# Optimization experiments

Hardware: AMD Instinct MI355X
Metric: run time of the kernel (lower is better)

Reference implementation:

```python
import jax, jax.numpy as jnp
import numpy as np


def _bilinear2d(uv, table):
    """Bilinear lookup with wrap addressing; sigmoid non-linearity applied per
    corner (normalize=True in SpatialGrid2D), matching training-time forward.
    uv: (N,2) in [0,1); table: (U,V,L). Returns (N,L)."""
    U, V, _ = table.shape
    su = uv[:, 0] * U
    sv = uv[:, 1] * V
    u0 = jnp.floor(su)
    v0 = jnp.floor(sv)
    fu = (su - u0)[:, None]  # fractional weights, (N,1)
    fv = (sv - v0)[:, None]
    u0i = jnp.mod(u0.astype(jnp.int32), U)
    v0i = jnp.mod(v0.astype(jnp.int32), V)
    u1i = jnp.mod(u0i + 1, U)
    v1i = jnp.mod(v0i + 1, V)
    t00 = jax.nn.sigmoid(table[u0i, v0i])
    t10 = jax.nn.sigmoid(table[u1i, v0i])
    t01 = jax.nn.sigmoid(table[u0i, v1i])
    t11 = jax.nn.sigmoid(table[u1i, v1i])
    return (t00 * (1 - fu) + t10 * fu) * (1 - fv) + (t01 * (1 - fu) + t11 * fu) * fv


def setup_inputs() -> dict:
    key = jax.random.key(0)
    k1, k2, k3 = jax.random.split(key, 3)
    N = 2048 * 2048  # query points (one per pixel)
    RES = 520        # grid0 resolution from nativeResolution=4096, compression=6
    x = jax.random.uniform(k1, (N, 2), dtype=jnp.float32)
    grid1_table = jax.random.normal(k2, (RES * 4, RES * 4, 2), dtype=jnp.float32)
    grid0_table = jax.random.normal(k3, (RES, RES, 3), dtype=jnp.float32)
    return {"x": x, "grid1_table": grid1_table, "grid0_table": grid0_table}


def reference(x, grid1_table, grid0_table):
    # forward: grid0(grid1(x)) -- chained bilinear indirection lookups
    key = _bilinear2d(x, grid1_table)   # (N,2) indirected uv coords in (0,1)
    return _bilinear2d(key, grid0_table)  # (N,3) decoded RGB
```

## Files before the change

### kernel.cpp

```cpp
#include <hip/hip_runtime.h>
#include <math.h>


__device__ __forceinline__ float mul_rn_nocontract(float a, float b) {
    float r;
    asm("v_mul_f32 %0, %1, %2" : "=v"(r) : "v"(a), "v"(b));
    return r;
}

__device__ __forceinline__ float sigmoid_f64(float t) {
    double e = exp(-(double)t);
    return (float)(1.0 / (1.0 + e));
}

__device__ __forceinline__ float sigmoid_fast(float t) {
    return 1.0f / (1.0f + __expf(-t));
}

__global__ void __launch_bounds__(256) sigmoid_table_kernel(
    const float4* __restrict__ in, float4* __restrict__ out, int n4)
{
    int i = blockIdx.x * blockDim.x + threadIdx.x;
    if (i >= n4) return;
    float4 v = in[i];
    float4 r;
    r.x = sigmoid_f64(v.x);
    r.y = sigmoid_f64(v.y);
    r.z = sigmoid_f64(v.z);
    r.w = sigmoid_f64(v.w);
    out[i] = r;
}

__global__ void __launch_bounds__(256) query_kernel(
    const float* __restrict__ x,
    const float* __restrict__ s1,
    const float* __restrict__ s0,
    float* __restrict__ out,
    int N, int U1, int U0)
{
    int i = blockIdx.x * blockDim.x + threadIdx.x;
    if (i >= N) return;

    float2 uv = reinterpret_cast<const float2*>(x)[i];

    float fU1 = (float)U1;
    float su = mul_rn_nocontract(uv.x, fU1);
    float sv = mul_rn_nocontract(uv.y, fU1);
    float u0f = floorf(su), v0f = floorf(sv);
    float fu = su - u0f;
    float fv = sv - v0f;
    int u0 = (int)u0f % U1; if (u0 < 0) u0 += U1;
    int v0 = (int)v0f % U1; if (v0 < 0) v0 += U1;
    int u1 = u0 + 1; if (u1 >= U1) u1 = 0;
    int v1 = v0 + 1; if (v1 >= U1) v1 = 0;

    const float2* s1v = reinterpret_cast<const float2*>(s1);
    float2 t00 = s1v[u0 * U1 + v0];
    float2 t10 = s1v[u1 * U1 + v0];
    float2 t01 = s1v[u0 * U1 + v1];
    float2 t11 = s1v[u1 * U1 + v1];

    float omfu = 1.0f - fu, omfv = 1.0f - fv;
    float kx = (t00.x * omfu + t10.x * fu) * omfv
             + (t01.x * omfu + t11.x * fu) * fv;
    float ky = (t00.y * omfu + t10.y * fu) * omfv
             + (t01.y * omfu + t11.y * fu) * fv;

    float fU0 = (float)U0;
    float su2 = mul_rn_nocontract(kx, fU0);
    float sv2 = mul_rn_nocontract(ky, fU0);
    float u0f2 = floorf(su2), v0f2 = floorf(sv2);
    float fu2 = su2 - u0f2;
    float fv2 = sv2 - v0f2;
    int p0 = (int)u0f2 % U0; if (p0 < 0) p0 += U0;
    int q0 = (int)v0f2 % U0; if (q0 < 0) q0 += U0;
    int p1 = p0 + 1; if (p1 >= U0) p1 = 0;
    int q1 = q0 + 1; if (q1 >= U0) q1 = 0;

    int b00 = (p0 * U0 + q0) * 3;
    int b10 = (p1 * U0 + q0) * 3;
    int b01 = (p0 * U0 + q1) * 3;
    int b11 = (p1 * U0 + q1) * 3;

    float omfu2 = 1.0f - fu2, omfv2 = 1.0f - fv2;

    float r0 = (s0[b00 + 0] * omfu2 + s0[b10 + 0] * fu2) * omfv2
             + (s0[b01 + 0] * omfu2 + s0[b11 + 0] * fu2) * fv2;
    float r1 = (s0[b00 + 1] * omfu2 + s0[b10 + 1] * fu2) * omfv2
             + (s0[b01 + 1] * omfu2 + s0[b11 + 1] * fu2) * fv2;
    float r2 = (s0[b00 + 2] * omfu2 + s0[b10 + 2] * fu2) * omfv2
             + (s0[b01 + 2] * omfu2 + s0[b11 + 2] * fu2) * fv2;

    out[3 * i + 0] = r0;
    out[3 * i + 1] = r1;
    out[3 * i + 2] = r2;
}

__global__ void __launch_bounds__(256) query_kernel_fallback(
    const float* __restrict__ x,
    const float* __restrict__ g1,
    const float* __restrict__ g0,
    float* __restrict__ out,
    int N, int U1, int U0)
{
    int i = blockIdx.x * blockDim.x + threadIdx.x;
    if (i >= N) return;

    float2 uv = reinterpret_cast<const float2*>(x)[i];

    float fU1 = (float)U1;
    float su = mul_rn_nocontract(uv.x, fU1);
    float sv = mul_rn_nocontract(uv.y, fU1);
    float u0f = floorf(su), v0f = floorf(sv);
    float fu = su - u0f, fv = sv - v0f;
    int u0 = (int)u0f % U1; if (u0 < 0) u0 += U1;
    int v0 = (int)v0f % U1; if (v0 < 0) v0 += U1;
    int u1 = u0 + 1; if (u1 >= U1) u1 = 0;
    int v1 = v0 + 1; if (v1 >= U1) v1 = 0;

    const float2* g1v = reinterpret_cast<const float2*>(g1);
    float2 t00 = g1v[u0 * U1 + v0];
    float2 t10 = g1v[u1 * U1 + v0];
    float2 t01 = g1v[u0 * U1 + v1];
    float2 t11 = g1v[u1 * U1 + v1];

    float a00x = sigmoid_f64(t00.x), a00y = sigmoid_f64(t00.y);
    float a10x = sigmoid_f64(t10.x), a10y = sigmoid_f64(t10.y);
    float a01x = sigmoid_f64(t01.x), a01y = sigmoid_f64(t01.y);
    float a11x = sigmoid_f64(t11.x), a11y = sigmoid_f64(t11.y);

    float omfu = 1.0f - fu, omfv = 1.0f - fv;
    float kx = (a00x * omfu + a10x * fu) * omfv + (a01x * omfu + a11x * fu) * fv;
    float ky = (a00y * omfu + a10y * fu) * omfv + (a01y * omfu + a11y * fu) * fv;

    float fU0 = (float)U0;
    float su2 = mul_rn_nocontract(kx, fU0);
    float sv2 = mul_rn_nocontract(ky, fU0);
    float u0f2 = floorf(su2), v0f2 = floorf(sv2);
    float fu2 = su2 - u0f2, fv2 = sv2 - v0f2;
    int p0 = (int)u0f2 % U0; if (p0 < 0) p0 += U0;
    int q0 = (int)v0f2 % U0; if (q0 < 0) q0 += U0;
    int p1 = p0 + 1; if (p1 >= U0) p1 = 0;
    int q1 = q0 + 1; if (q1 >= U0) q1 = 0;

    int b00 = (p0 * U0 + q0) * 3;
    int b10 = (p1 * U0 + q0) * 3;
    int b01 = (p0 * U0 + q1) * 3;
    int b11 = (p1 * U0 + q1) * 3;

    float omfu2 = 1.0f - fu2, omfv2 = 1.0f - fv2;
    float r0 = (sigmoid_fast(g0[b00+0]) * omfu2 + sigmoid_fast(g0[b10+0]) * fu2) * omfv2
             + (sigmoid_fast(g0[b01+0]) * omfu2 + sigmoid_fast(g0[b11+0]) * fu2) * fv2;
    float r1 = (sigmoid_fast(g0[b00+1]) * omfu2 + sigmoid_fast(g0[b10+1]) * fu2) * omfv2
             + (sigmoid_fast(g0[b01+1]) * omfu2 + sigmoid_fast(g0[b11+1]) * fu2) * fv2;
    float r2 = (sigmoid_fast(g0[b00+2]) * omfu2 + sigmoid_fast(g0[b10+2]) * fu2) * omfv2
             + (sigmoid_fast(g0[b01+2]) * omfu2 + sigmoid_fast(g0[b11+2]) * fu2) * fv2;

    out[3 * i + 0] = r0;
    out[3 * i + 1] = r1;
    out[3 * i + 2] = r2;
}

extern "C" void kernel_launch(void* const* d_in, const int* in_sizes, int n_in,
                              void* d_out, int out_size, void* d_ws, size_t ws_size,
                              hipStream_t stream) {
    const float* x  = (const float*)d_in[0];
    const float* g1 = (const float*)d_in[1];
    const float* g0 = (const float*)d_in[2];
    float* out = (float*)d_out;

    int N = in_sizes[0] / 2;
    long long n1 = in_sizes[1];
    long long n0 = in_sizes[2];
    int U1 = (int)(sqrt((double)(n1 / 2)) + 0.5);
    int U0 = (int)(sqrt((double)(n0 / 3)) + 0.5);

    size_t need = (size_t)(n1 + n0) * sizeof(float);
    int block = 256;
    int qgrid = (N + block - 1) / block;

    if (ws_size >= need && (n1 % 4) == 0 && (n0 % 4) == 0) {
        float* s1 = (float*)d_ws;
        float* s0 = s1 + n1;
        int n1_4 = (int)(n1 / 4), n0_4 = (int)(n0 / 4);
        sigmoid_table_kernel<<<(n1_4 + block - 1) / block, block, 0, stream>>>(
            (const float4*)g1, (float4*)s1, n1_4);
        sigmoid_table_kernel<<<(n0_4 + block - 1) / block, block, 0, stream>>>(
            (const float4*)g0, (float4*)s0, n0_4);
        query_kernel<<<qgrid, block, 0, stream>>>(x, s1, s0, out, N, U1, U0);
    } else {
        query_kernel_fallback<<<qgrid, block, 0, stream>>>(x, g1, g0, out, N, U1, U0);
    }
}
```

Before: 287.0 us.

## Pad grid0 sigmoid table to float4 and process two queries per thread

Precomputes the grid0 sigmoid table padded to one float4 per cell, so each corner needs a single vector gather instead of three scalar loads. Grid1 corners are fetched as float4 pairs covering adjacent v cells, with a small fix-up branch when v wraps around. Each thread now handles two query points, with nontemporal vector loads of the inputs and nontemporal stores of the outputs. This is meant to cut gather instruction count and raise memory-level parallelism, at the cost of extra workspace, 8-byte-aligned float4 loads and higher register pressure.

```diff
diff --git a/kernel.cpp b/kernel.cpp
--- a/kernel.cpp
+++ b/kernel.cpp
@@ -1,6 +1,9 @@
 #include <hip/hip_runtime.h>
 #include <math.h>
 
+
+typedef float f32x2 __attribute__((ext_vector_type(2)));
+typedef float f32x4 __attribute__((ext_vector_type(4)));
 
 __device__ __forceinline__ float mul_rn_nocontract(float a, float b) {
     float r;
@@ -31,7 +34,133 @@
     out[i] = r;
 }
 
-__global__ void __launch_bounds__(256) query_kernel(
+__global__ void __launch_bounds__(256) sigmoid_pad_kernel(
+    const float* __restrict__ g0, float4* __restrict__ s0p, int ncells)
+{
+    int j = blockIdx.x * blockDim.x + threadIdx.x;
+    if (j >= ncells) return;
+    float a = g0[3 * j + 0];
+    float b = g0[3 * j + 1];
+    float c = g0[3 * j + 2];
+    s0p[j] = make_float4(sigmoid_f64(a), sigmoid_f64(b), sigmoid_f64(c), 0.0f);
+}
+
+__global__ void __launch_bounds__(256) query2_kernel(
+    const float* __restrict__ x,
+    const float* __restrict__ s1,
+    const float4* __restrict__ s0p,
+    float* __restrict__ out,
+    int N, int U1, int U0)
+{
+    int t = blockIdx.x * blockDim.x + threadIdx.x;
+    int i0 = t * 2;
+    if (i0 >= N) return;
+    bool two = (i0 + 1 < N);
+
+    f32x4 xv = __builtin_nontemporal_load(reinterpret_cast<const f32x4*>(x) + t);
+    if (!two) { xv.z = xv.x; xv.w = xv.y; }
+
+    float ux[2] = {xv.x, xv.z};
+    float uy[2] = {xv.y, xv.w};
+
+    float fU1 = (float)U1;
+    int cA[2], cB[2];
+    bool vwrap[2];
+    float fu[2], fv[2];
+#pragma unroll
+    for (int p = 0; p < 2; ++p) {
+        float su = mul_rn_nocontract(ux[p], fU1);
+        float sv = mul_rn_nocontract(uy[p], fU1);
+        float u0f = floorf(su), v0f = floorf(sv);
+        fu[p] = su - u0f;
+        fv[p] = sv - v0f;
+        int u0 = (int)u0f % U1; if (u0 < 0) u0 += U1;
+        int v0 = (int)v0f % U1; if (v0 < 0) v0 += U1;
+        int u1 = u0 + 1; if (u1 >= U1) u1 = 0;
+        vwrap[p] = (v0 == U1 - 1);
+        cA[p] = u0 * U1 + v0;
+        cB[p] = u1 * U1 + v0;
+    }
+
+    float4 rA[2], rB[2];
+#pragma unroll
+    for (int p = 0; p < 2; ++p) {
+        rA[p] = *reinterpret_cast<const float4*>(s1 + 2 * cA[p]);
+        rB[p] = *reinterpret_cast<const float4*>(s1 + 2 * cB[p]);
+    }
+
+    float kx[2], ky[2];
+    const float2* s1v = reinterpret_cast<const float2*>(s1);
+#pragma unroll
+    for (int p = 0; p < 2; ++p) {
+        if (vwrap[p]) {
+            float2 c01 = s1v[cA[p] - (U1 - 1)];
+            float2 c11 = s1v[cB[p] - (U1 - 1)];
+            rA[p].z = c01.x; rA[p].w = c01.y;
+            rB[p].z = c11.x; rB[p].w = c11.y;
+        }
+        float omfu = 1.0f - fu[p], omfv = 1.0f - fv[p];
+        kx[p] = (rA[p].x * omfu + rB[p].x * fu[p]) * omfv
+              + (rA[p].z * omfu + rB[p].z * fu[p]) * fv[p];
+        ky[p] = (rA[p].y * omfu + rB[p].y * fu[p]) * omfv
+              + (rA[p].w * omfu + rB[p].w * fu[p]) * fv[p];
+    }
+
+    float fU0 = (float)U0;
+    int b00[2], b10[2], b01[2], b11[2];
+    float fu2[2], fv2[2];
+#pragma unroll
+    for (int p = 0; p < 2; ++p) {
+        float su2 = mul_rn_nocontract(kx[p], fU0);
+        float sv2 = mul_rn_nocontract(ky[p], fU0);
+        float u0f2 = floorf(su2), v0f2 = floorf(sv2);
+        fu2[p] = su2 - u0f2;
+        fv2[p] = sv2 - v0f2;
+        int p0 = (int)u0f2 % U0; if (p0 < 0) p0 += U0;
+        int q0 = (int)v0f2 % U0; if (q0 < 0) q0 += U0;
+        int p1 = p0 + 1; if (p1 >= U0) p1 = 0;
+        int q1 = q0 + 1; if (q1 >= U0) q1 = 0;
+        b00[p] = p0 * U0 + q0;
+        b10[p] = p1 * U0 + q0;
+        b01[p] = p0 * U0 + q1;
+        b11[p] = p1 * U0 + q1;
+    }
+
+    float4 c00[2], c10[2], c01[2], c11[2];
+#pragma unroll
+    for (int p = 0; p < 2; ++p) {
+        c00[p] = s0p[b00[p]];
+        c10[p] = s0p[b10[p]];
+        c01[p] = s0p[b01[p]];
+        c11[p] = s0p[b11[p]];
+    }
+
+    float res[6];
+#pragma unroll
+    for (int p = 0; p < 2; ++p) {
+        float omfu2 = 1.0f - fu2[p], omfv2 = 1.0f - fv2[p];
+        res[3*p+0] = (c00[p].x * omfu2 + c10[p].x * fu2[p]) * omfv2
+                   + (c01[p].x * omfu2 + c11[p].x * fu2[p]) * fv2[p];
+        res[3*p+1] = (c00[p].y * omfu2 + c10[p].y * fu2[p]) * omfv2
+                   + (c01[p].y * omfu2 + c11[p].y * fu2[p]) * fv2[p];
+        res[3*p+2] = (c00[p].z * omfu2 + c10[p].z * fu2[p]) * omfv2
+                   + (c01[p].z * omfu2 + c11[p].z * fu2[p]) * fv2[p];
+    }
+
+    float* op = out + (size_t)i0 * 3;
+    if (two) {
+        f32x2 s0v = {res[0], res[1]};
+        f32x2 s1v2 = {res[2], res[3]};
+        f32x2 s2v = {res[4], res[5]};
+        __builtin_nontemporal_store(s0v, reinterpret_cast<f32x2*>(op));
+        __builtin_nontemporal_store(s1v2, reinterpret_cast<f32x2*>(op + 2));
+        __builtin_nontemporal_store(s2v, reinterpret_cast<f32x2*>(op + 4));
+    } else {
+        op[0] = res[0]; op[1] = res[1]; op[2] = res[2];
+    }
+}
+
+__global__ void __launch_bounds__(256) query_kernel_unpadded(
     const float* __restrict__ x,
     const float* __restrict__ s1,
     const float* __restrict__ s0,
@@ -40,74 +169,7 @@
 {
     int i = blockIdx.x * blockDim.x + threadIdx.x;
     if (i >= N) return;
-
     float2 uv = reinterpret_cast<const float2*>(x)[i];
-
-    float fU1 = (float)U1;
-    float su = mul_rn_nocontract(uv.x, fU1);
-    float sv = mul_rn_nocontract(uv.y, fU1);
-    float u0f = floorf(su), v0f = floorf(sv);
-    float fu = su - u0f;
-    float fv = sv - v0f;
-    int u0 = (int)u0f % U1; if (u0 < 0) u0 += U1;
-    int v0 = (int)v0f % U1; if (v0 < 0) v0 += U1;
-    int u1 = u0 + 1; if (u1 >= U1) u1 = 0;
-    int v1 = v0 + 1; if (v1 >= U1) v1 = 0;
-
-    const float2* s1v = reinterpret_cast<const float2*>(s1);
-    float2 t00 = s1v[u0 * U1 + v0];
-    float2 t10 = s1v[u1 * U1 + v0];
-    float2 t01 = s1v[u0 * U1 + v1];
-    float2 t11 = s1v[u1 * U1 + v1];
-
-    float omfu = 1.0f - fu, omfv = 1.0f - fv;
-    float kx = (t00.x * omfu + t10.x * fu) * omfv
-             + (t01.x * omfu + t11.x * fu) * fv;
-    float ky = (t00.y * omfu + t10.y * fu) * omfv
-             + (t01.y * omfu + t11.y * fu) * fv;
-
-    float fU0 = (float)U0;
-    float su2 = mul_rn_nocontract(kx, fU0);
-    float sv2 = mul_rn_nocontract(ky, fU0);
-    float u0f2 = floorf(su2), v0f2 = floorf(sv2);
-    float fu2 = su2 - u0f2;
-    float fv2 = sv2 - v0f2;
-    int p0 = (int)u0f2 % U0; if (p0 < 0) p0 += U0;
-    int q0 = (int)v0f2 % U0; if (q0 < 0) q0 += U0;
-    int p1 = p0 + 1; if (p1 >= U0) p1 = 0;
-    int q1 = q0 + 1; if (q1 >= U0) q1 = 0;
-
-    int b00 = (p0 * U0 + q0) * 3;
-    int b10 = (p1 * U0 + q0) * 3;
-    int b01 = (p0 * U0 + q1) * 3;
-    int b11 = (p1 * U0 + q1) * 3;
-
-    float omfu2 = 1.0f - fu2, omfv2 = 1.0f - fv2;
-
-    float r0 = (s0[b00 + 0] * omfu2 + s0[b10 + 0] * fu2) * omfv2
-             + (s0[b01 + 0] * omfu2 + s0[b11 + 0] * fu2) * fv2;
-    float r1 = (s0[b00 + 1] * omfu2 + s0[b10 + 1] * fu2) * omfv2
-             + (s0[b01 + 1] * omfu2 + s0[b11 + 1] * fu2) * fv2;
-    float r2 = (s0[b00 + 2] * omfu2 + s0[b10 + 2] * fu2) * omfv2
-             + (s0[b01 + 2] * omfu2 + s0[b11 + 2] * fu2) * fv2;
-
-    out[3 * i + 0] = r0;
-    out[3 * i + 1] = r1;
-    out[3 * i + 2] = r2;
-}
-
-__global__ void __launch_bounds__(256) query_kernel_fallback(
-    const float* __restrict__ x,
-    const float* __restrict__ g1,
-    const float* __restrict__ g0,
-    float* __restrict__ out,
-    int N, int U1, int U0)
-{
-    int i = blockIdx.x * blockDim.x + threadIdx.x;
-    if (i >= N) return;
-
-    float2 uv = reinterpret_cast<const float2*>(x)[i];
-
     float fU1 = (float)U1;
     float su = mul_rn_nocontract(uv.x, fU1);
     float sv = mul_rn_nocontract(uv.y, fU1);
@@ -117,22 +179,14 @@
     int v0 = (int)v0f % U1; if (v0 < 0) v0 += U1;
     int u1 = u0 + 1; if (u1 >= U1) u1 = 0;
     int v1 = v0 + 1; if (v1 >= U1) v1 = 0;
-
-    const float2* g1v = reinterpret_cast<const float2*>(g1);
-    float2 t00 = g1v[u0 * U1 + v0];
-    float2 t10 = g1v[u1 * U1 + v0];
-    float2 t01 = g1v[u0 * U1 + v1];
-    float2 t11 = g1v[u1 * U1 + v1];
-
-    float a00x = sigmoid_f64(t00.x), a00y = sigmoid_f64(t00.y);
-    float a10x = sigmoid_f64(t10.x), a10y = sigmoid_f64(t10.y);
-    float a01x = sigmoid_f64(t01.x), a01y = sigmoid_f64(t01.y);
-    float a11x = sigmoid_f64(t11.x), a11y = sigmoid_f64(t11.y);
-
+    const float2* s1v = reinterpret_cast<const float2*>(s1);
+    float2 t00 = s1v[u0 * U1 + v0];
+    float2 t10 = s1v[u1 * U1 + v0];
+    float2 t01 = s1v[u0 * U1 + v1];
+    float2 t11 = s1v[u1 * U1 + v1];
     float omfu = 1.0f - fu, omfv = 1.0f - fv;
-    float kx = (a00x * omfu + a10x * fu) * omfv + (a01x * omfu + a11x * fu) * fv;
-    float ky = (a00y * omfu + a10y * fu) * omfv + (a01y * omfu + a11y * fu) * fv;
-
+    float kx = (t00.x * omfu + t10.x * fu) * omfv + (t01.x * omfu + t11.x * fu) * fv;
+    float ky = (t00.y * omfu + t10.y * fu) * omfv + (t01.y * omfu + t11.y * fu) * fv;
     float fU0 = (float)U0;
     float su2 = mul_rn_nocontract(kx, fU0);
     float sv2 = mul_rn_nocontract(ky, fU0);
@@ -142,12 +196,60 @@
     int q0 = (int)v0f2 % U0; if (q0 < 0) q0 += U0;
     int p1 = p0 + 1; if (p1 >= U0) p1 = 0;
     int q1 = q0 + 1; if (q1 >= U0) q1 = 0;
-
-    int b00 = (p0 * U0 + q0) * 3;
-    int b10 = (p1 * U0 + q0) * 3;
-    int b01 = (p0 * U0 + q1) * 3;
-    int b11 = (p1 * U0 + q1) * 3;
-
+    int b00 = (p0 * U0 + q0) * 3, b10 = (p1 * U0 + q0) * 3;
+    int b01 = (p0 * U0 + q1) * 3, b11 = (p1 * U0 + q1) * 3;
+    float omfu2 = 1.0f - fu2, omfv2 = 1.0f - fv2;
+    float r0 = (s0[b00+0] * omfu2 + s0[b10+0] * fu2) * omfv2
+             + (s0[b01+0] * omfu2 + s0[b11+0] * fu2) * fv2;
+    float r1 = (s0[b00+1] * omfu2 + s0[b10+1] * fu2) * omfv2
+             + (s0[b01+1] * omfu2 + s0[b11+1] * fu2) * fv2;
+    float r2 = (s0[b00+2] * omfu2 + s0[b10+2] * fu2) * omfv2
+             + (s0[b01+2] * omfu2 + s0[b11+2] * fu2) * fv2;
+    out[3*i+0] = r0; out[3*i+1] = r1; out[3*i+2] = r2;
+}
+
+__global__ void __launch_bounds__(256) query_kernel_fallback(
+    const float* __restrict__ x,
+    const float* __restrict__ g1,
+    const float* __restrict__ g0,
+    float* __restrict__ out,
+    int N, int U1, int U0)
+{
+    int i = blockIdx.x * blockDim.x + threadIdx.x;
+    if (i >= N) return;
+    float2 uv = reinterpret_cast<const float2*>(x)[i];
+    float fU1 = (float)U1;
+    float su = mul_rn_nocontract(uv.x, fU1);
+    float sv = mul_rn_nocontract(uv.y, fU1);
+    float u0f = floorf(su), v0f = floorf(sv);
+    float fu = su - u0f, fv = sv - v0f;
+    int u0 = (int)u0f % U1; if (u0 < 0) u0 += U1;
+    int v0 = (int)v0f % U1; if (v0 < 0) v0 += U1;
+    int u1 = u0 + 1; if (u1 >= U1) u1 = 0;
+    int v1 = v0 + 1; if (v1 >= U1) v1 = 0;
+    const float2* g1v = reinterpret_cast<const float2*>(g1);
+    float2 t00 = g1v[u0 * U1 + v0];
+    float2 t10 = g1v[u1 * U1 + v0];
+    float2 t01 = g1v[u0 * U1 + v1];
+    float2 t11 = g1v[u1 * U1 + v1];
+    float a00x = sigmoid_f64(t00.x), a00y = sigmoid_f64(t00.y);
+    float a10x = sigmoid_f64(t10.x), a10y = sigmoid_f64(t10.y);
+    float a01x = sigmoid_f64(t01.x), a01y = sigmoid_f64(t01.y);
+    float a11x = sigmoid_f64(t11.x), a11y = sigmoid_f64(t11.y);
+    float omfu = 1.0f - fu, omfv = 1.0f - fv;
+    float kx = (a00x * omfu + a10x * fu) * omfv + (a01x * omfu + a11x * fu) * fv;
+    float ky = (a00y * omfu + a10y * fu) * omfv + (a01y * omfu + a11y * fu) * fv;
+    float fU0 = (float)U0;
+    float su2 = mul_rn_nocontract(kx, fU0);
+    float sv2 = mul_rn_nocontract(ky, fU0);
+    float u0f2 = floorf(su2), v0f2 = floorf(sv2);
+    float fu2 = su2 - u0f2, fv2 = sv2 - v0f2;
+    int p0 = (int)u0f2 % U0; if (p0 < 0) p0 += U0;
+    int q0 = (int)v0f2 % U0; if (q0 < 0) q0 += U0;
+    int p1 = p0 + 1; if (p1 >= U0) p1 = 0;
+    int q1 = q0 + 1; if (q1 >= U0) q1 = 0;
+    int b00 = (p0 * U0 + q0) * 3, b10 = (p1 * U0 + q0) * 3;
+    int b01 = (p0 * U0 + q1) * 3, b11 = (p1 * U0 + q1) * 3;
     float omfu2 = 1.0f - fu2, omfv2 = 1.0f - fv2;
     float r0 = (sigmoid_fast(g0[b00+0]) * omfu2 + sigmoid_fast(g0[b10+0]) * fu2) * omfv2
              + (sigmoid_fast(g0[b01+0]) * omfu2 + sigmoid_fast(g0[b11+0]) * fu2) * fv2;
@@ -155,10 +257,7 @@
              + (sigmoid_fast(g0[b01+1]) * omfu2 + sigmoid_fast(g0[b11+1]) * fu2) * fv2;
     float r2 = (sigmoid_fast(g0[b00+2]) * omfu2 + sigmoid_fast(g0[b10+2]) * fu2) * omfv2
              + (sigmoid_fast(g0[b01+2]) * omfu2 + sigmoid_fast(g0[b11+2]) * fu2) * fv2;
-
-    out[3 * i + 0] = r0;
-    out[3 * i + 1] = r1;
-    out[3 * i + 2] = r2;
+    out[3*i+0] = r0; out[3*i+1] = r1; out[3*i+2] = r2;
 }
 
 extern "C" void kernel_launch(void* const* d_in, const int* in_sizes, int n_in,
@@ -174,12 +273,24 @@
     long long n0 = in_sizes[2];
     int U1 = (int)(sqrt((double)(n1 / 2)) + 0.5);
     int U0 = (int)(sqrt((double)(n0 / 3)) + 0.5);
-
-    size_t need = (size_t)(n1 + n0) * sizeof(float);
+    int ncells0 = U0 * U0;
+
     int block = 256;
-    int qgrid = (N + block - 1) / block;
-
-    if (ws_size >= need && (n1 % 4) == 0 && (n0 % 4) == 0) {
+    size_t need_pad   = ((size_t)n1 + (size_t)ncells0 * 4) * sizeof(float);
+    size_t need_plain = ((size_t)n1 + (size_t)n0) * sizeof(float);
+
+    if (ws_size >= need_pad && (n1 % 4) == 0 && (N % 2) == 0) {
+        float* s1 = (float*)d_ws;
+        float4* s0p = (float4*)(s1 + n1);
+        int n1_4 = (int)(n1 / 4);
+        sigmoid_table_kernel<<<(n1_4 + block - 1) / block, block, 0, stream>>>(
+            (const float4*)g1, (float4*)s1, n1_4);
+        sigmoid_pad_kernel<<<(ncells0 + block - 1) / block, block, 0, stream>>>(
+            g0, s0p, ncells0);
+        int nthreads = (N + 1) / 2;
+        query2_kernel<<<(nthreads + block - 1) / block, block, 0, stream>>>(
+            x, s1, s0p, out, N, U1, U0);
+    } else if (ws_size >= need_plain && (n1 % 4) == 0 && (n0 % 4) == 0) {
         float* s1 = (float*)d_ws;
         float* s0 = s1 + n1;
         int n1_4 = (int)(n1 / 4), n0_4 = (int)(n0 / 4);
@@ -187,8 +298,10 @@
             (const float4*)g1, (float4*)s1, n1_4);
         sigmoid_table_kernel<<<(n0_4 + block - 1) / block, block, 0, stream>>>(
             (const float4*)g0, (float4*)s0, n0_4);
-        query_kernel<<<qgrid, block, 0, stream>>>(x, s1, s0, out, N, U1, U0);
+        query_kernel_unpadded<<<(N + block - 1) / block, block, 0, stream>>>(
+            x, s1, s0, out, N, U1, U0);
     } else {
-        query_kernel_fallback<<<qgrid, block, 0, stream>>>(x, g1, g0, out, N, U1, U0);
-    }
-}
+        query_kernel_fallback<<<(N + block - 1) / block, block, 0, stream>>>(
+            x, g1, g0, out, N, U1, U0);
+    }
+}
```

New measurement: 332.6 us. 15.9% more time.

## Pack four bilinear corners per cell into contiguous sigmoid table

Applied to the files above, without the earlier changes.

A new preprocessing kernel builds a per-cell table holding the sigmoided values of all four wrap-addressed corners of grid1 (8 floats, 32 bytes), so each query does two adjacent float4 loads instead of four scattered float2 gathers. The query input load is also made nontemporal. The cost is a table four times larger (about 138 MB instead of 35 MB) built on every call, which adds write traffic and lowers cache hit rates for the random first-level lookups. The packed path runs only if the workspace is large enough, otherwise the previous path is used.

```diff
diff --git a/kernel.cpp b/kernel.cpp
--- a/kernel.cpp
+++ b/kernel.cpp
@@ -1,6 +1,9 @@
 #include <hip/hip_runtime.h>
 #include <math.h>
 
+
+typedef float f32x2 __attribute__((ext_vector_type(2)));
+typedef float f32x4 __attribute__((ext_vector_type(4)));
 
 __device__ __forceinline__ float mul_rn_nocontract(float a, float b) {
     float r;
@@ -31,9 +34,33 @@
     out[i] = r;
 }
 
-__global__ void __launch_bounds__(256) query_kernel(
+__global__ void __launch_bounds__(256) pack_corners_kernel(
+    const float* __restrict__ g1, float* __restrict__ pk, int U1)
+{
+    int c = blockIdx.x * blockDim.x + threadIdx.x;
+    int ncells = U1 * U1;
+    if (c >= ncells) return;
+    int u = c / U1;
+    int v = c - u * U1;
+    int u1 = (u + 1 == U1) ? 0 : u + 1;
+    int v1 = (v + 1 == U1) ? 0 : v + 1;
+    const float2* g = reinterpret_cast<const float2*>(g1);
+    float2 a = g[u * U1 + v];
+    float2 b = g[u * U1 + v1];
+    float2 d = g[u1 * U1 + v];
+    float2 e = g[u1 * U1 + v1];
+    float4 lo = make_float4(sigmoid_f64(a.x), sigmoid_f64(a.y),
+                            sigmoid_f64(b.x), sigmoid_f64(b.y));
+    float4 hi = make_float4(sigmoid_f64(d.x), sigmoid_f64(d.y),
+                            sigmoid_f64(e.x), sigmoid_f64(e.y));
+    float4* o = reinterpret_cast<float4*>(pk + (size_t)c * 8);
+    o[0] = lo;
+    o[1] = hi;
+}
+
+__global__ void __launch_bounds__(256) query_packed_kernel(
     const float* __restrict__ x,
-    const float* __restrict__ s1,
+    const float* __restrict__ pk,
     const float* __restrict__ s0,
     float* __restrict__ out,
     int N, int U1, int U0)
@@ -41,7 +68,8 @@
     int i = blockIdx.x * blockDim.x + threadIdx.x;
     if (i >= N) return;
 
-    float2 uv = reinterpret_cast<const float2*>(x)[i];
+    f32x2 uv = __builtin_nontemporal_load(
+        reinterpret_cast<const f32x2*>(x) + i);
 
     float fU1 = (float)U1;
     float su = mul_rn_nocontract(uv.x, fU1);
@@ -51,63 +79,49 @@
     float fv = sv - v0f;
     int u0 = (int)u0f % U1; if (u0 < 0) u0 += U1;
     int v0 = (int)v0f % U1; if (v0 < 0) v0 += U1;
-    int u1 = u0 + 1; if (u1 >= U1) u1 = 0;
-    int v1 = v0 + 1; if (v1 >= U1) v1 = 0;
-
-    const float2* s1v = reinterpret_cast<const float2*>(s1);
-    float2 t00 = s1v[u0 * U1 + v0];
-    float2 t10 = s1v[u1 * U1 + v0];
-    float2 t01 = s1v[u0 * U1 + v1];
-    float2 t11 = s1v[u1 * U1 + v1];
+
+    const float4* cell = reinterpret_cast<const float4*>(pk)
+                       + (size_t)(u0 * U1 + v0) * 2;
+    float4 lo = cell[0];
+    float4 hi = cell[1];
 
     float omfu = 1.0f - fu, omfv = 1.0f - fv;
-    float kx = (t00.x * omfu + t10.x * fu) * omfv
-             + (t01.x * omfu + t11.x * fu) * fv;
-    float ky = (t00.y * omfu + t10.y * fu) * omfv
-             + (t01.y * omfu + t11.y * fu) * fv;
+    float kx = (lo.x * omfu + hi.x * fu) * omfv
+             + (lo.z * omfu + hi.z * fu) * fv;
+    float ky = (lo.y * omfu + hi.y * fu) * omfv
+             + (lo.w * omfu + hi.w * fu) * fv;
 
     float fU0 = (float)U0;
     float su2 = mul_rn_nocontract(kx, fU0);
     float sv2 = mul_rn_nocontract(ky, fU0);
     float u0f2 = floorf(su2), v0f2 = floorf(sv2);
-    float fu2 = su2 - u0f2;
-    float fv2 = sv2 - v0f2;
+    float fu2 = su2 - u0f2, fv2 = sv2 - v0f2;
     int p0 = (int)u0f2 % U0; if (p0 < 0) p0 += U0;
     int q0 = (int)v0f2 % U0; if (q0 < 0) q0 += U0;
     int p1 = p0 + 1; if (p1 >= U0) p1 = 0;
     int q1 = q0 + 1; if (q1 >= U0) q1 = 0;
-
-    int b00 = (p0 * U0 + q0) * 3;
-    int b10 = (p1 * U0 + q0) * 3;
-    int b01 = (p0 * U0 + q1) * 3;
-    int b11 = (p1 * U0 + q1) * 3;
-
+    int b00 = (p0 * U0 + q0) * 3, b10 = (p1 * U0 + q0) * 3;
+    int b01 = (p0 * U0 + q1) * 3, b11 = (p1 * U0 + q1) * 3;
     float omfu2 = 1.0f - fu2, omfv2 = 1.0f - fv2;
-
-    float r0 = (s0[b00 + 0] * omfu2 + s0[b10 + 0] * fu2) * omfv2
-             + (s0[b01 + 0] * omfu2 + s0[b11 + 0] * fu2) * fv2;
-    float r1 = (s0[b00 + 1] * omfu2 + s0[b10 + 1] * fu2) * omfv2
-             + (s0[b01 + 1] * omfu2 + s0[b11 + 1] * fu2) * fv2;
-    float r2 = (s0[b00 + 2] * omfu2 + s0[b10 + 2] * fu2) * omfv2
-             + (s0[b01 + 2] * omfu2 + s0[b11 + 2] * fu2) * fv2;
-
-    out[3 * i + 0] = r0;
-    out[3 * i + 1] = r1;
-    out[3 * i + 2] = r2;
-}
-
-__global__ void __launch_bounds__(256) query_kernel_fallback(
+    float r0 = (s0[b00+0] * omfu2 + s0[b10+0] * fu2) * omfv2
+             + (s0[b01+0] * omfu2 + s0[b11+0] * fu2) * fv2;
+    float r1 = (s0[b00+1] * omfu2 + s0[b10+1] * fu2) * omfv2
+             + (s0[b01+1] * omfu2 + s0[b11+1] * fu2) * fv2;
+    float r2 = (s0[b00+2] * omfu2 + s0[b10+2] * fu2) * omfv2
+             + (s0[b01+2] * omfu2 + s0[b11+2] * fu2) * fv2;
+    out[3*i+0] = r0; out[3*i+1] = r1; out[3*i+2] = r2;
+}
+
+__global__ void __launch_bounds__(256) query_kernel_unpadded(
     const float* __restrict__ x,
-    const float* __restrict__ g1,
-    const float* __restrict__ g0,
+    const float* __restrict__ s1,
+    const float* __restrict__ s0,
     float* __restrict__ out,
     int N, int U1, int U0)
 {
     int i = blockIdx.x * blockDim.x + threadIdx.x;
     if (i >= N) return;
-
     float2 uv = reinterpret_cast<const float2*>(x)[i];
-
     float fU1 = (float)U1;
     float su = mul_rn_nocontract(uv.x, fU1);
     float sv = mul_rn_nocontract(uv.y, fU1);
@@ -117,22 +131,14 @@
     int v0 = (int)v0f % U1; if (v0 < 0) v0 += U1;
     int u1 = u0 + 1; if (u1 >= U1) u1 = 0;
     int v1 = v0 + 1; if (v1 >= U1) v1 = 0;
-
-    const float2* g1v = reinterpret_cast<const float2*>(g1);
-    float2 t00 = g1v[u0 * U1 + v0];
-    float2 t10 = g1v[u1 * U1 + v0];
-    float2 t01 = g1v[u0 * U1 + v1];
-    float2 t11 = g1v[u1 * U1 + v1];
-
-    float a00x = sigmoid_f64(t00.x), a00y = sigmoid_f64(t00.y);
-    float a10x = sigmoid_f64(t10.x), a10y = sigmoid_f64(t10.y);
-    float a01x = sigmoid_f64(t01.x), a01y = sigmoid_f64(t01.y);
-    float a11x = sigmoid_f64(t11.x), a11y = sigmoid_f64(t11.y);
-
+    const float2* s1v = reinterpret_cast<const float2*>(s1);
+    float2 t00 = s1v[u0 * U1 + v0];
+    float2 t10 = s1v[u1 * U1 + v0];
+    float2 t01 = s1v[u0 * U1 + v1];
+    float2 t11 = s1v[u1 * U1 + v1];
     float omfu = 1.0f - fu, omfv = 1.0f - fv;
-    float kx = (a00x * omfu + a10x * fu) * omfv + (a01x * omfu + a11x * fu) * fv;
-    float ky = (a00y * omfu + a10y * fu) * omfv + (a01y * omfu + a11y * fu) * fv;
-
+    float kx = (t00.x * omfu + t10.x * fu) * omfv + (t01.x * omfu + t11.x * fu) * fv;
+    float ky = (t00.y * omfu + t10.y * fu) * omfv + (t01.y * omfu + t11.y * fu) * fv;
     float fU0 = (float)U0;
     float su2 = mul_rn_nocontract(kx, fU0);
     float sv2 = mul_rn_nocontract(ky, fU0);
@@ -142,12 +148,60 @@
     int q0 = (int)v0f2 % U0; if (q0 < 0) q0 += U0;
     int p1 = p0 + 1; if (p1 >= U0) p1 = 0;
     int q1 = q0 + 1; if (q1 >= U0) q1 = 0;
-
-    int b00 = (p0 * U0 + q0) * 3;
-    int b10 = (p1 * U0 + q0) * 3;
-    int b01 = (p0 * U0 + q1) * 3;
-    int b11 = (p1 * U0 + q1) * 3;
-
+    int b00 = (p0 * U0 + q0) * 3, b10 = (p1 * U0 + q0) * 3;
+    int b01 = (p0 * U0 + q1) * 3, b11 = (p1 * U0 + q1) * 3;
+    float omfu2 = 1.0f - fu2, omfv2 = 1.0f - fv2;
+    float r0 = (s0[b00+0] * omfu2 + s0[b10+0] * fu2) * omfv2
+             + (s0[b01+0] * omfu2 + s0[b11+0] * fu2) * fv2;
+    float r1 = (s0[b00+1] * omfu2 + s0[b10+1] * fu2) * omfv2
+             + (s0[b01+1] * omfu2 + s0[b11+1] * fu2) * fv2;
+    float r2 = (s0[b00+2] * omfu2 + s0[b10+2] * fu2) * omfv2
+             + (s0[b01+2] * omfu2 + s0[b11+2] * fu2) * fv2;
+    out[3*i+0] = r0; out[3*i+1] = r1; out[3*i+2] = r2;
+}
+
+__global__ void __launch_bounds__(256) query_kernel_fallback(
+    const float* __restrict__ x,
+    const float* __restrict__ g1,
+    const float* __restrict__ g0,
+    float* __restrict__ out,
+    int N, int U1, int U0)
+{
+    int i = blockIdx.x * blockDim.x + threadIdx.x;
+    if (i >= N) return;
+    float2 uv = reinterpret_cast<const float2*>(x)[i];
+    float fU1 = (float)U1;
+    float su = mul_rn_nocontract(uv.x, fU1);
+    float sv = mul_rn_nocontract(uv.y, fU1);
+    float u0f = floorf(su), v0f = floorf(sv);
+    float fu = su - u0f, fv = sv - v0f;
+    int u0 = (int)u0f % U1; if (u0 < 0) u0 += U1;
+    int v0 = (int)v0f % U1; if (v0 < 0) v0 += U1;
+    int u1 = u0 + 1; if (u1 >= U1) u1 = 0;
+    int v1 = v0 + 1; if (v1 >= U1) v1 = 0;
+    const float2* g1v = reinterpret_cast<const float2*>(g1);
+    float2 t00 = g1v[u0 * U1 + v0];
+    float2 t10 = g1v[u1 * U1 + v0];
+    float2 t01 = g1v[u0 * U1 + v1];
+    float2 t11 = g1v[u1 * U1 + v1];
+    float a00x = sigmoid_f64(t00.x), a00y = sigmoid_f64(t00.y);
+    float a10x = sigmoid_f64(t10.x), a10y = sigmoid_f64(t10.y);
+    float a01x = sigmoid_f64(t01.x), a01y = sigmoid_f64(t01.y);
+    float a11x = sigmoid_f64(t11.x), a11y = sigmoid_f64(t11.y);
+    float omfu = 1.0f - fu, omfv = 1.0f - fv;
+    float kx = (a00x * omfu + a10x * fu) * omfv + (a01x * omfu + a11x * fu) * fv;
+    float ky = (a00y * omfu + a10y * fu) * omfv + (a01y * omfu + a11y * fu) * fv;
+    float fU0 = (float)U0;
+    float su2 = mul_rn_nocontract(kx, fU0);
+    float sv2 = mul_rn_nocontract(ky, fU0);
+    float u0f2 = floorf(su2), v0f2 = floorf(sv2);
+    float fu2 = su2 - u0f2, fv2 = sv2 - v0f2;
+    int p0 = (int)u0f2 % U0; if (p0 < 0) p0 += U0;
+    int q0 = (int)v0f2 % U0; if (q0 < 0) q0 += U0;
+    int p1 = p0 + 1; if (p1 >= U0) p1 = 0;
+    int q1 = q0 + 1; if (q1 >= U0) q1 = 0;
+    int b00 = (p0 * U0 + q0) * 3, b10 = (p1 * U0 + q0) * 3;
+    int b01 = (p0 * U0 + q1) * 3, b11 = (p1 * U0 + q1) * 3;
     float omfu2 = 1.0f - fu2, omfv2 = 1.0f - fv2;
     float r0 = (sigmoid_fast(g0[b00+0]) * omfu2 + sigmoid_fast(g0[b10+0]) * fu2) * omfv2
              + (sigmoid_fast(g0[b01+0]) * omfu2 + sigmoid_fast(g0[b11+0]) * fu2) * fv2;
@@ -155,10 +209,7 @@
              + (sigmoid_fast(g0[b01+1]) * omfu2 + sigmoid_fast(g0[b11+1]) * fu2) * fv2;
     float r2 = (sigmoid_fast(g0[b00+2]) * omfu2 + sigmoid_fast(g0[b10+2]) * fu2) * omfv2
              + (sigmoid_fast(g0[b01+2]) * omfu2 + sigmoid_fast(g0[b11+2]) * fu2) * fv2;
-
-    out[3 * i + 0] = r0;
-    out[3 * i + 1] = r1;
-    out[3 * i + 2] = r2;
+    out[3*i+0] = r0; out[3*i+1] = r1; out[3*i+2] = r2;
 }
 
 extern "C" void kernel_launch(void* const* d_in, const int* in_sizes, int n_in,
@@ -174,12 +225,23 @@
     long long n0 = in_sizes[2];
     int U1 = (int)(sqrt((double)(n1 / 2)) + 0.5);
     int U0 = (int)(sqrt((double)(n0 / 3)) + 0.5);
-
-    size_t need = (size_t)(n1 + n0) * sizeof(float);
+    long long ncells1 = (long long)U1 * U1;
+
     int block = 256;
-    int qgrid = (N + block - 1) / block;
-
-    if (ws_size >= need && (n1 % 4) == 0 && (n0 % 4) == 0) {
+    size_t need_packed = ((size_t)ncells1 * 8 + (size_t)n0) * sizeof(float);
+    size_t need_plain  = ((size_t)n1 + (size_t)n0) * sizeof(float);
+
+    if (ws_size >= need_packed && (n0 % 4) == 0) {
+        float* pk = (float*)d_ws;
+        float* s0 = pk + ncells1 * 8;
+        int n0_4 = (int)(n0 / 4);
+        pack_corners_kernel<<<(int)((ncells1 + block - 1) / block), block, 0, stream>>>(
+            g1, pk, U1);
+        sigmoid_table_kernel<<<(n0_4 + block - 1) / block, block, 0, stream>>>(
+            (const float4*)g0, (float4*)s0, n0_4);
+        query_packed_kernel<<<(N + block - 1) / block, block, 0, stream>>>(
+            x, pk, s0, out, N, U1, U0);
+    } else if (ws_size >= need_plain && (n1 % 4) == 0 && (n0 % 4) == 0) {
         float* s1 = (float*)d_ws;
         float* s0 = s1 + n1;
         int n1_4 = (int)(n1 / 4), n0_4 = (int)(n0 / 4);
@@ -187,8 +249,10 @@
             (const float4*)g1, (float4*)s1, n1_4);
         sigmoid_table_kernel<<<(n0_4 + block - 1) / block, block, 0, stream>>>(
             (const float4*)g0, (float4*)s0, n0_4);
-        query_kernel<<<qgrid, block, 0, stream>>>(x, s1, s0, out, N, U1, U0);
+        query_kernel_unpadded<<<(N + block - 1) / block, block, 0, stream>>>(
+            x, s1, s0, out, N, U1, U0);
     } else {
-        query_kernel_fallback<<<qgrid, block, 0, stream>>>(x, g1, g0, out, N, U1, U0);
+        query_kernel_fallback<<<(N + block - 1) / block, block, 0, stream>>>(
+            x, g1, g0, out, N, U1, U0);
     }
 }
```

New measurement: 263.8 us. -8.1%, faster.
